# Kernel optimization log

Measured on AMD Instinct MI355X. Metric: run time of the kernel, lower is better.

## Reference

```python
import jax, jax.numpy as jnp
import numpy as np

GRID = (160, 160, 160)
RADIUS_FACTOR = 3.0
PATCH = 20      # fixed patch edge; covers ceil(c+r)-floor(c-r)+1 for r <= 9 voxels
CHUNK = 500
N_POINTS = 25000


def _quat_to_rot(q):
    # normalized quaternion -> rotation matrix (matches torch reference)
    q = q / jnp.clip(jnp.linalg.norm(q, axis=-1, keepdims=True), 1e-6)
    w, x, y, z = q[..., 0], q[..., 1], q[..., 2], q[..., 3]
    ww, xx, yy, zz = w * w, x * x, y * y, z * z
    wx, wy, wz = w * x, w * y, w * z
    xy, xz, yz = x * y, x * z, y * z
    r0 = jnp.stack([ww + xx - yy - zz, 2 * (xy - wz), 2 * (xz + wy)], -1)
    r1 = jnp.stack([2 * (xy + wz), ww - xx + yy - zz, 2 * (yz - wx)], -1)
    r2 = jnp.stack([2 * (xz - wy), 2 * (yz + wx), ww - xx - yy + zz], -1)
    return jnp.stack([r0, r1, r2], -2)


def setup_inputs():
    key = jax.random.key(0)
    k1, k2, k3, k4 = jax.random.split(key, 4)
    centers = jax.random.uniform(k1, (N_POINTS, 3), dtype=jnp.float32)
    # scales in [1.5, 3.0] voxels -> patch radius = 3*max(scale) <= 9 < PATCH/2
    log_scales = jnp.log(jax.random.uniform(k2, (N_POINTS, 3), minval=1.5, maxval=3.0, dtype=jnp.float32))
    quats = jax.random.normal(k3, (N_POINTS, 4), dtype=jnp.float32)
    rho = 0.1 * jax.random.normal(k4, (N_POINTS, 2), dtype=jnp.float32)  # (real, imag)
    return {"centers": centers, "log_scales": log_scales, "quats": quats, "rho": rho}


def _splat(centers, log_scales, quats, rho):
    D, H, W = GRID
    span = jnp.array([D - 1, H - 1, W - 1], jnp.float32)
    scales = jnp.exp(log_scales)                                  # [N,3]
    R = _quat_to_rot(quats)                                       # [N,3,3]
    inv = 1.0 / jnp.clip(scales, 1e-4) ** 2                       # diag of S^-2
    prec = jnp.einsum('nij,nj,nkj->nik', R, inv, R)               # R diag R^T, [N,3,3]
    cv = centers * span                                           # voxel-space centers
    rad = jnp.max(scales, axis=-1) * RADIUS_FACTOR                # per-point patch radius
    base = jnp.floor(cv - rad[:, None]).astype(jnp.int32)         # zmin/ymin/xmin (pre-clip)
    hi = jnp.ceil(cv + rad[:, None]).astype(jnp.int32)            # zmax/ymax/xmax (pre-clip)
    amp_mag = jnp.sqrt(rho[:, 0] ** 2 + rho[:, 1] ** 2)
    valid = (amp_mag >= 1e-6) & (rad >= 1e-3)                     # torch skip conditions
    dims = jnp.array([D, H, W], jnp.int32)

    nchunk = N_POINTS // CHUNK
    ck = lambda a: a.reshape((nchunk, CHUNK) + a.shape[1:])
    xs = (ck(cv), ck(base), ck(hi), ck(prec), ck(rho), ck(valid))
    offs = jnp.arange(PATCH, dtype=jnp.int32)

    def step(vol, x):
        cv_c, base_c, hi_c, p, rho_c, val_c = x
        idx = base_c[:, :, None] + offs                           # [C,3,P] voxel indices
        d = idx.astype(jnp.float32) - cv_c[:, :, None]            # [C,3,P] rel coords
        m = (idx >= 0) & (idx < dims[None, :, None]) & (idx <= hi_c[:, :, None])
        dz, dy, dx = d[:, 0], d[:, 1], d[:, 2]                    # [C,P] each
        # exponent = rel^T prec rel, built separably (prec is symmetric)
        e = ((p[:, 0, 0, None] * dz * dz)[:, :, None, None]
             + (p[:, 1, 1, None] * dy * dy)[:, None, :, None]
             + (p[:, 2, 2, None] * dx * dx)[:, None, None, :]
             + (2.0 * p[:, 0, 1, None, None] * dz[:, :, None] * dy[:, None, :])[:, :, :, None]
             + (2.0 * p[:, 0, 2, None, None] * dz[:, :, None] * dx[:, None, :])[:, :, None, :]
             + (2.0 * p[:, 1, 2, None, None] * dy[:, :, None] * dx[:, None, :])[:, None, :, :])
        w = jnp.exp(-0.5 * e)                                     # [C,P,P,P]
        mask = (m[:, 0, :, None, None] & m[:, 1, None, :, None] & m[:, 2, None, None, :]
                & val_c[:, None, None, None])
        w = jnp.where(mask, w, 0.0)
        iz = jnp.clip(idx[:, 0], 0, D - 1)
        iy = jnp.clip(idx[:, 1], 0, H - 1)
        ix = jnp.clip(idx[:, 2], 0, W - 1)
        lin = (iz[:, :, None, None] * H + iy[:, None, :, None]) * W + ix[:, None, None, :]
        contrib = w[..., None] * rho_c[:, None, None, None, :]    # [C,P,P,P,2] (re,im)
        vol = vol.at[lin.reshape(-1)].add(contrib.reshape(-1, 2))
        return vol, None

    vol, _ = jax.lax.scan(step, jnp.zeros((D * H * W, 2), jnp.float32), xs)
    return vol.reshape(D, H, W, 2)


def reference(centers, log_scales, quats, rho):
    return _splat(centers, log_scales, quats, rho)
```

## Files before the change

kernel.cpp:

```cpp
#include <hip/hip_runtime.h>


namespace {
constexpr int GD = 160, GH = 160, GW = 160;
constexpr int NPTS = 25000;
constexpr int PATCH = 20;
constexpr int TS  = 8;
constexpr int TPD = GD / TS;
constexpr int NT  = TPD * TPD * TPD;
constexpr int CAP = 384;
constexpr int PSTRIDE = 20;
constexpr float L2E = 1.4426950408889634f;
}

typedef float f32x2 __attribute__((ext_vector_type(2)));

__device__ __forceinline__ f32x2 pk_mul(f32x2 a, f32x2 b) {
    f32x2 d;
    asm("v_pk_mul_f32 %0, %1, %2" : "=v"(d) : "v"(a), "v"(b));
    return d;
}
__device__ __forceinline__ f32x2 pk_fma(f32x2 a, f32x2 b, f32x2 c) {
    f32x2 d;
    asm("v_pk_fma_f32 %0, %1, %2, %3" : "=v"(d) : "v"(a), "v"(b), "v"(c));
    return d;
}


__global__ __launch_bounds__(256) void prep_bin(
    const float* __restrict__ centers,
    const float* __restrict__ log_scales,
    const float* __restrict__ quats,
    const float* __restrict__ rho,
    float* __restrict__ params,
    int* __restrict__ counts,
    unsigned short* __restrict__ list)
{
    const int t = blockIdx.x * 256 + threadIdx.x;
    const int gid  = t >> 6;
    const int lane = t & 63;

    const float r0 = rho[gid * 2 + 0];
    const float r1 = rho[gid * 2 + 1];
    const float s0 = __expf(log_scales[gid * 3 + 0]);
    const float s1 = __expf(log_scales[gid * 3 + 1]);
    const float s2 = __expf(log_scales[gid * 3 + 2]);

    const float smax = fmaxf(s0, fmaxf(s1, s2));
    const float rad  = smax * 3.0f;
    const float amp2 = r0 * r0 + r1 * r1;

    const float cvz = centers[gid * 3 + 0] * (float)(GD - 1);
    const float cvy = centers[gid * 3 + 1] * (float)(GH - 1);
    const float cvx = centers[gid * 3 + 2] * (float)(GW - 1);

    const int bz = (int)floorf(cvz - rad);
    const int by = (int)floorf(cvy - rad);
    const int bx = (int)floorf(cvx - rad);
    const int hz = (int)ceilf(cvz + rad);
    const int hy = (int)ceilf(cvy + rad);
    const int hx = (int)ceilf(cvx + rad);

    const int loz = max(bz, 0), upz = min(min(hz, GD - 1), bz + PATCH - 1);
    const int loy = max(by, 0), upy = min(min(hy, GH - 1), by + PATCH - 1);
    const int lox = max(bx, 0), upx = min(min(hx, GW - 1), bx + PATCH - 1);

    const bool valid = (amp2 >= 1e-12f) && (rad >= 1e-3f) &&
                       (upz >= loz) && (upy >= loy) && (upx >= lox);

    const float q0 = quats[gid * 4 + 0], q1 = quats[gid * 4 + 1];
    const float q2 = quats[gid * 4 + 2], q3 = quats[gid * 4 + 3];
    float qn = sqrtf(q0 * q0 + q1 * q1 + q2 * q2 + q3 * q3);
    qn = fmaxf(qn, 1e-6f);
    const float w = q0 / qn, x = q1 / qn, y = q2 / qn, z = q3 / qn;

    const float R00 = w * w + x * x - y * y - z * z;
    const float R01 = 2.f * (x * y - w * z);
    const float R02 = 2.f * (x * z + w * y);
    const float R10 = 2.f * (x * y + w * z);
    const float R11 = w * w - x * x + y * y - z * z;
    const float R12 = 2.f * (y * z - w * x);
    const float R20 = 2.f * (x * z - w * y);
    const float R21 = 2.f * (y * z + w * x);
    const float R22 = w * w - x * x - y * y + z * z;

    const float c0 = fmaxf(s0, 1e-4f); const float i0 = 1.f / (c0 * c0);
    const float c1 = fmaxf(s1, 1e-4f); const float i1 = 1.f / (c1 * c1);
    const float c2 = fmaxf(s2, 1e-4f); const float i2 = 1.f / (c2 * c2);

    const float p00 = R00 * R00 * i0 + R01 * R01 * i1 + R02 * R02 * i2;
    const float p01 = R00 * R10 * i0 + R01 * R11 * i1 + R02 * R12 * i2;
    const float p02 = R00 * R20 * i0 + R01 * R21 * i1 + R02 * R22 * i2;
    const float p11 = R10 * R10 * i0 + R11 * R11 * i1 + R12 * R12 * i2;
    const float p12 = R10 * R20 * i0 + R11 * R21 * i1 + R12 * R22 * i2;
    const float p22 = R20 * R20 * i0 + R21 * R21 * i1 + R22 * R22 * i2;

    const float q00s = -0.5f * L2E * p00;
    const float v    = __builtin_amdgcn_exp2f(2.f * q00s);
    const float v2   = v * v;
    const float v4   = v2 * v2;

    const int zl = valid ? loz : 255, zu = valid ? upz : 0;
    const int yl = valid ? loy : 255, yu = valid ? upy : 0;
    const int xl = valid ? lox : 255, xu = valid ? upx : 0;
    const int loPack = zl | (yl << 8) | (xl << 16) | (zu << 24);
    const int upPack = yu | (xu << 8);

    if (lane == 0) {
        float4* P = reinterpret_cast<float4*>(params + (size_t)gid * PSTRIDE);
        P[0] = make_float4(q00s, -L2E * p01, -L2E * p02, -0.5f * L2E * p11);
        P[1] = make_float4(-L2E * p12, -0.5f * L2E * p22, cvz, cvy);
        P[2] = make_float4(cvx, __int_as_float(loPack), __int_as_float(upPack), v);
        P[3] = make_float4(r0, r0, r1, r1);
        P[4] = make_float4(v2, 0.f, v4, v4);
    }

    if (!valid) return;

    const int tz0 = loz >> 3, tz1 = upz >> 3;
    const int ty0 = loy >> 3, ty1 = upy >> 3;
    const int tx0 = lox >> 3, tx1 = upx >> 3;
    const int tz = tz0 + (lane >> 4);
    const int ty = ty0 + ((lane >> 2) & 3);
    const int tx = tx0 + (lane & 3);
    if (tz > tz1 || ty > ty1 || tx > tx1) return;
    const int tile = (tz * TPD + ty) * TPD + tx;
    const int pos = atomicAdd(&counts[tile], 1);
    if (pos < CAP) list[(size_t)tile * CAP + pos] = (unsigned short)gid;
}

__global__ __launch_bounds__(256, 6) void gather(
    const float* __restrict__ params,
    const int* __restrict__ counts,
    const unsigned short* __restrict__ list,
    float2* __restrict__ out)
{
    const int wli  = threadIdx.x >> 6;
    const int lane = threadIdx.x & 63;
    const int tile = blockIdx.x * 4 + wli;
    const int tz = tile / (TPD * TPD);
    const int rem = tile - tz * (TPD * TPD);
    const int ty = rem / TPD;
    const int tx = rem - ty * TPD;

    const int ly = lane >> 3, lx = lane & 7;
    const int iy = ty * TS + ly;
    const int ix = tx * TS + lx;
    const int z0 = tz * TS;
    const float fy = (float)iy, fx = (float)ix, fz = (float)z0;

    __shared__ float4 sP[4][64][5];

    int cnt = __builtin_amdgcn_readfirstlane(counts[tile]);
    if (cnt > CAP) cnt = CAP;
    const float4* p4 = reinterpret_cast<const float4*>(params);
    const unsigned short* tl = list + (size_t)tile * CAP;

    f32x2 Ar[4], Ai[4];
#pragma unroll
    for (int i = 0; i < 4; ++i) {
        Ar[i].x = 0.f; Ar[i].y = 0.f;
        Ai[i].x = 0.f; Ai[i].y = 0.f;
    }

    for (int b0 = 0; b0 < cnt; b0 += 64) {
        const int nb = min(64, cnt - b0);
        if (lane < nb) {
            const int g = tl[b0 + lane];
            const float4* src = p4 + (size_t)g * 5;
            sP[wli][lane][0] = src[0];
            sP[wli][lane][1] = src[1];
            sP[wli][lane][2] = src[2];
            sP[wli][lane][3] = src[3];
            sP[wli][lane][4] = src[4];
        }
        for (int g = 0; g < nb; ++g) {
            const float4 Pa = sP[wli][g][0];
            const float4 Pb = sP[wli][g][1];
            const float4 Pc = sP[wli][g][2];
            const float4 Pd = sP[wli][g][3];
            const float4 Pe = sP[wli][g][4];
            const int lo = __builtin_amdgcn_readfirstlane(__float_as_int(Pc.y));
            const int up = __builtin_amdgcn_readfirstlane(__float_as_int(Pc.z));
            const int loy_ = (lo >> 8) & 255, lox_ = (lo >> 16) & 255;
            const int upy_ = up & 255,        upx_ = (up >> 8) & 255;
            const int zl = (lo & 255) - z0;
            const int zu = ((lo >> 24) & 255) - z0;
            const bool yx = (iy >= loy_) & (iy <= upy_) &
                            (ix >= lox_) & (ix <= upx_);

            const float dy = fy - Pb.w;
            const float dx = fx - Pc.x;
            const float C = fmaf(dy, fmaf(Pa.w, dy, Pb.x * dx), Pb.y * dx * dx);
            const float B = fmaf(Pa.y, dy, Pa.z * dx);
            const float dz = fz - Pb.z;
            const float t0 = fmaf(dz, fmaf(Pa.x, dz, B), C);
            const float dt = fmaf(Pa.x, fmaf(2.f, dz, 1.f), B);
            const float w0 = __builtin_amdgcn_exp2f(t0);
            const float u0 = __builtin_amdgcn_exp2f(dt);
            const float w0m = yx ? w0 : 0.f;

            const float s0 = u0 * u0 * Pc.w;
            const float s1 = s0 * Pe.x;
            f32x2 W;  W.x = w0m; W.y = w0m * u0;
            f32x2 S;  S.x = s0;  S.y = s1;
            f32x2 R0; R0.x = Pd.x; R0.y = Pd.y;
            f32x2 R1; R1.x = Pd.z; R1.y = Pd.w;
            f32x2 V4; V4.x = Pe.z; V4.y = Pe.w;

            if (zl <= 0 && zu >= 7) {
#pragma unroll
                for (int k = 0; k < 4; ++k) {
                    Ar[k] = pk_fma(W, R0, Ar[k]);
                    Ai[k] = pk_fma(W, R1, Ai[k]);
                    if (k < 3) { W = pk_mul(W, S); S = pk_mul(S, V4); }
                }
            } else {
#pragma unroll
                for (int k = 0; k < 4; ++k) {
                    f32x2 WM;
                    WM.x = (2 * k     >= zl && 2 * k     <= zu) ? W.x : 0.f;
                    WM.y = (2 * k + 1 >= zl && 2 * k + 1 <= zu) ? W.y : 0.f;
                    Ar[k] = pk_fma(WM, R0, Ar[k]);
                    Ai[k] = pk_fma(WM, R1, Ai[k]);
                    if (k < 3) { W = pk_mul(W, S); S = pk_mul(S, V4); }
                }
            }
        }
    }

#pragma unroll
    for (int k = 0; k < 4; ++k) {
        out[((size_t)(z0 + 2 * k)     * GH + iy) * GW + ix] =
            make_float2(Ar[k].x, Ai[k].x);
        out[((size_t)(z0 + 2 * k + 1) * GH + iy) * GW + ix] =
            make_float2(Ar[k].y, Ai[k].y);
    }
}

extern "C" void kernel_launch(void* const* d_in, const int* in_sizes, int n_in,
                              void* d_out, int out_size, void* d_ws, size_t ws_size,
                              hipStream_t stream) {
    const float* centers    = (const float*)d_in[0];
    const float* log_scales = (const float*)d_in[1];
    const float* quats      = (const float*)d_in[2];
    const float* rho        = (const float*)d_in[3];

    float* params = (float*)d_ws;
    int* counts = (int*)(params + (size_t)NPTS * PSTRIDE);
    unsigned short* list = (unsigned short*)(counts + NT);

    hipMemsetAsync(counts, 0, NT * sizeof(int), stream);
    prep_bin<<<(NPTS * 64) / 256, 256, 0, stream>>>(centers, log_scales, quats,
                                                    rho, params, counts, list);
    gather<<<NT / 4, 256, 0, stream>>>(params, counts, list, (float2*)d_out);
}
```

Baseline: 167.7 us.

## Schedule gather tiles via persistent workers pulling heavy tiles first

Adds a small kernel that partitions tiles into a queue, with tiles above a point-count threshold at the front and light tiles at the back. The gather kernel becomes persistent: a fixed grid of waves pulls tiles from the queue with an atomic counter, so heavy tiles start early and light ones fill the tail. This targets load imbalance across tiles with very different list lengths. It costs an extra launch, one global atomic per tile, and an unordered split within each class.

```diff
diff --git a/kernel.cpp b/kernel.cpp
--- a/kernel.cpp
+++ b/kernel.cpp
@@ -10,6 +10,7 @@
 constexpr int NT  = TPD * TPD * TPD;
 constexpr int CAP = 384;
 constexpr int PSTRIDE = 20;
+constexpr int HEAVY_THR = 96;
 constexpr float L2E = 1.4426950408889634f;
 }
 
@@ -129,112 +130,136 @@
     if (pos < CAP) list[(size_t)tile * CAP + pos] = (unsigned short)gid;
 }
 
+__global__ __launch_bounds__(256) void make_queue(
+    const int* __restrict__ counts,
+    int* __restrict__ queue,
+    int* __restrict__ qc)
+{
+    const int t = blockIdx.x * 256 + threadIdx.x;
+    if (t >= NT) return;
+    if (counts[t] > HEAVY_THR) {
+        queue[atomicAdd(&qc[0], 1)] = t;
+    } else {
+        queue[NT - 1 - atomicAdd(&qc[1], 1)] = t;
+    }
+}
+
 __global__ __launch_bounds__(256, 6) void gather(
     const float* __restrict__ params,
     const int* __restrict__ counts,
     const unsigned short* __restrict__ list,
+    const int* __restrict__ queue,
+    int* __restrict__ qc,
     float2* __restrict__ out)
 {
     const int wli  = threadIdx.x >> 6;
     const int lane = threadIdx.x & 63;
-    const int tile = blockIdx.x * 4 + wli;
-    const int tz = tile / (TPD * TPD);
-    const int rem = tile - tz * (TPD * TPD);
-    const int ty = rem / TPD;
-    const int tx = rem - ty * TPD;
-
-    const int ly = lane >> 3, lx = lane & 7;
-    const int iy = ty * TS + ly;
-    const int ix = tx * TS + lx;
-    const int z0 = tz * TS;
-    const float fy = (float)iy, fx = (float)ix, fz = (float)z0;
 
     __shared__ float4 sP[4][64][5];
-
-    int cnt = __builtin_amdgcn_readfirstlane(counts[tile]);
-    if (cnt > CAP) cnt = CAP;
     const float4* p4 = reinterpret_cast<const float4*>(params);
-    const unsigned short* tl = list + (size_t)tile * CAP;
-
-    f32x2 Ar[4], Ai[4];
-#pragma unroll
-    for (int i = 0; i < 4; ++i) {
-        Ar[i].x = 0.f; Ar[i].y = 0.f;
-        Ai[i].x = 0.f; Ai[i].y = 0.f;
-    }
-
-    for (int b0 = 0; b0 < cnt; b0 += 64) {
-        const int nb = min(64, cnt - b0);
-        if (lane < nb) {
-            const int g = tl[b0 + lane];
-            const float4* src = p4 + (size_t)g * 5;
-            sP[wli][lane][0] = src[0];
-            sP[wli][lane][1] = src[1];
-            sP[wli][lane][2] = src[2];
-            sP[wli][lane][3] = src[3];
-            sP[wli][lane][4] = src[4];
+
+    for (;;) {
+        int pos0 = 0;
+        if (lane == 0) pos0 = atomicAdd(&qc[2], 1);
+        const int pos = __shfl(pos0, 0);
+        if (pos >= NT) break;
+        const int tile = __builtin_amdgcn_readfirstlane(queue[pos]);
+
+        const int tz = tile / (TPD * TPD);
+        const int rem = tile - tz * (TPD * TPD);
+        const int ty = rem / TPD;
+        const int tx = rem - ty * TPD;
+
+        const int ly = lane >> 3, lx = lane & 7;
+        const int iy = ty * TS + ly;
+        const int ix = tx * TS + lx;
+        const int z0 = tz * TS;
+        const float fy = (float)iy, fx = (float)ix, fz = (float)z0;
+
+        int cnt = __builtin_amdgcn_readfirstlane(counts[tile]);
+        if (cnt > CAP) cnt = CAP;
+        const unsigned short* tl = list + (size_t)tile * CAP;
+
+        f32x2 Ar[4], Ai[4];
+#pragma unroll
+        for (int i = 0; i < 4; ++i) {
+            Ar[i].x = 0.f; Ar[i].y = 0.f;
+            Ai[i].x = 0.f; Ai[i].y = 0.f;
         }
-        for (int g = 0; g < nb; ++g) {
-            const float4 Pa = sP[wli][g][0];
-            const float4 Pb = sP[wli][g][1];
-            const float4 Pc = sP[wli][g][2];
-            const float4 Pd = sP[wli][g][3];
-            const float4 Pe = sP[wli][g][4];
-            const int lo = __builtin_amdgcn_readfirstlane(__float_as_int(Pc.y));
-            const int up = __builtin_amdgcn_readfirstlane(__float_as_int(Pc.z));
-            const int loy_ = (lo >> 8) & 255, lox_ = (lo >> 16) & 255;
-            const int upy_ = up & 255,        upx_ = (up >> 8) & 255;
-            const int zl = (lo & 255) - z0;
-            const int zu = ((lo >> 24) & 255) - z0;
-            const bool yx = (iy >= loy_) & (iy <= upy_) &
-                            (ix >= lox_) & (ix <= upx_);
-
-            const float dy = fy - Pb.w;
-            const float dx = fx - Pc.x;
-            const float C = fmaf(dy, fmaf(Pa.w, dy, Pb.x * dx), Pb.y * dx * dx);
-            const float B = fmaf(Pa.y, dy, Pa.z * dx);
-            const float dz = fz - Pb.z;
-            const float t0 = fmaf(dz, fmaf(Pa.x, dz, B), C);
-            const float dt = fmaf(Pa.x, fmaf(2.f, dz, 1.f), B);
-            const float w0 = __builtin_amdgcn_exp2f(t0);
-            const float u0 = __builtin_amdgcn_exp2f(dt);
-            const float w0m = yx ? w0 : 0.f;
-
-            const float s0 = u0 * u0 * Pc.w;
-            const float s1 = s0 * Pe.x;
-            f32x2 W;  W.x = w0m; W.y = w0m * u0;
-            f32x2 S;  S.x = s0;  S.y = s1;
-            f32x2 R0; R0.x = Pd.x; R0.y = Pd.y;
-            f32x2 R1; R1.x = Pd.z; R1.y = Pd.w;
-            f32x2 V4; V4.x = Pe.z; V4.y = Pe.w;
-
-            if (zl <= 0 && zu >= 7) {
-#pragma unroll
-                for (int k = 0; k < 4; ++k) {
-                    Ar[k] = pk_fma(W, R0, Ar[k]);
-                    Ai[k] = pk_fma(W, R1, Ai[k]);
-                    if (k < 3) { W = pk_mul(W, S); S = pk_mul(S, V4); }
-                }
-            } else {
-#pragma unroll
-                for (int k = 0; k < 4; ++k) {
-                    f32x2 WM;
-                    WM.x = (2 * k     >= zl && 2 * k     <= zu) ? W.x : 0.f;
-                    WM.y = (2 * k + 1 >= zl && 2 * k + 1 <= zu) ? W.y : 0.f;
-                    Ar[k] = pk_fma(WM, R0, Ar[k]);
-                    Ai[k] = pk_fma(WM, R1, Ai[k]);
-                    if (k < 3) { W = pk_mul(W, S); S = pk_mul(S, V4); }
+
+        for (int b0 = 0; b0 < cnt; b0 += 64) {
+            const int nb = min(64, cnt - b0);
+            if (lane < nb) {
+                const int g = tl[b0 + lane];
+                const float4* src = p4 + (size_t)g * 5;
+                sP[wli][lane][0] = src[0];
+                sP[wli][lane][1] = src[1];
+                sP[wli][lane][2] = src[2];
+                sP[wli][lane][3] = src[3];
+                sP[wli][lane][4] = src[4];
+            }
+            for (int g = 0; g < nb; ++g) {
+                const float4 Pa = sP[wli][g][0];
+                const float4 Pb = sP[wli][g][1];
+                const float4 Pc = sP[wli][g][2];
+                const float4 Pd = sP[wli][g][3];
+                const float4 Pe = sP[wli][g][4];
+                const int lo = __builtin_amdgcn_readfirstlane(__float_as_int(Pc.y));
+                const int up = __builtin_amdgcn_readfirstlane(__float_as_int(Pc.z));
+                const int loy_ = (lo >> 8) & 255, lox_ = (lo >> 16) & 255;
+                const int upy_ = up & 255,        upx_ = (up >> 8) & 255;
+                const int zl = (lo & 255) - z0;
+                const int zu = ((lo >> 24) & 255) - z0;
+                const bool yx = (iy >= loy_) & (iy <= upy_) &
+                                (ix >= lox_) & (ix <= upx_);
+
+                const float dy = fy - Pb.w;
+                const float dx = fx - Pc.x;
+                const float C = fmaf(dy, fmaf(Pa.w, dy, Pb.x * dx), Pb.y * dx * dx);
+                const float B = fmaf(Pa.y, dy, Pa.z * dx);
+                const float dz = fz - Pb.z;
+                const float t0 = fmaf(dz, fmaf(Pa.x, dz, B), C);
+                const float dt = fmaf(Pa.x, fmaf(2.f, dz, 1.f), B);
+                const float w0 = __builtin_amdgcn_exp2f(t0);
+                const float u0 = __builtin_amdgcn_exp2f(dt);
+                const float w0m = yx ? w0 : 0.f;
+
+                const float s0 = u0 * u0 * Pc.w;
+                const float s1 = s0 * Pe.x;
+                f32x2 W;  W.x = w0m; W.y = w0m * u0;
+                f32x2 S;  S.x = s0;  S.y = s1;
+                f32x2 R0; R0.x = Pd.x; R0.y = Pd.y;
+                f32x2 R1; R1.x = Pd.z; R1.y = Pd.w;
+                f32x2 V4; V4.x = Pe.z; V4.y = Pe.w;
+
+                if (zl <= 0 && zu >= 7) {
+#pragma unroll
+                    for (int k = 0; k < 4; ++k) {
+                        Ar[k] = pk_fma(W, R0, Ar[k]);
+                        Ai[k] = pk_fma(W, R1, Ai[k]);
+                        if (k < 3) { W = pk_mul(W, S); S = pk_mul(S, V4); }
+                    }
+                } else {
+#pragma unroll
+                    for (int k = 0; k < 4; ++k) {
+                        f32x2 WM;
+                        WM.x = (2 * k     >= zl && 2 * k     <= zu) ? W.x : 0.f;
+                        WM.y = (2 * k + 1 >= zl && 2 * k + 1 <= zu) ? W.y : 0.f;
+                        Ar[k] = pk_fma(WM, R0, Ar[k]);
+                        Ai[k] = pk_fma(WM, R1, Ai[k]);
+                        if (k < 3) { W = pk_mul(W, S); S = pk_mul(S, V4); }
+                    }
                 }
             }
         }
-    }
-
-#pragma unroll
-    for (int k = 0; k < 4; ++k) {
-        out[((size_t)(z0 + 2 * k)     * GH + iy) * GW + ix] =
-            make_float2(Ar[k].x, Ai[k].x);
-        out[((size_t)(z0 + 2 * k + 1) * GH + iy) * GW + ix] =
-            make_float2(Ar[k].y, Ai[k].y);
+
+#pragma unroll
+        for (int k = 0; k < 4; ++k) {
+            out[((size_t)(z0 + 2 * k)     * GH + iy) * GW + ix] =
+                make_float2(Ar[k].x, Ai[k].x);
+            out[((size_t)(z0 + 2 * k + 1) * GH + iy) * GW + ix] =
+                make_float2(Ar[k].y, Ai[k].y);
+        }
     }
 }
 
@@ -248,10 +273,14 @@
 
     float* params = (float*)d_ws;
     int* counts = (int*)(params + (size_t)NPTS * PSTRIDE);
-    unsigned short* list = (unsigned short*)(counts + NT);
-
-    hipMemsetAsync(counts, 0, NT * sizeof(int), stream);
+    int* qc     = counts + NT;
+    int* queue  = qc + 4;
+    unsigned short* list = (unsigned short*)(queue + NT);
+
+    hipMemsetAsync(counts, 0, (NT + 4) * sizeof(int), stream);
     prep_bin<<<(NPTS * 64) / 256, 256, 0, stream>>>(centers, log_scales, quats,
                                                     rho, params, counts, list);
-    gather<<<NT / 4, 256, 0, stream>>>(params, counts, list, (float2*)d_out);
-}
+    make_queue<<<(NT + 255) / 256, 256, 0, stream>>>(counts, queue, qc);
+    gather<<<2048, 256, 0, stream>>>(params, counts, list, queue, qc,
+                                     (float2*)d_out);
+}
```

Result: slower. 306.2 us (+82.6%).

## Replace LDS staging with register-prefetched uniform param loads in gather

Applied to the files above, without the earlier changes.

Shrinks the per-point parameter record from 20 to 16 floats by dropping duplicated fields. The gather kernel no longer stages batches of parameters in shared memory. Each wave now loads one point's parameters straight from global memory (wave-uniform addresses), with software pipelining that fetches the next point's record and the index after that one while the current point is computed. This removes the LDS writes and reads and the staging phase. The cost is more global/L2 load latency on the critical path and more registers held for the prefetch.

```diff
diff --git a/kernel.cpp b/kernel.cpp
--- a/kernel.cpp
+++ b/kernel.cpp
@@ -9,7 +9,7 @@
 constexpr int TPD = GD / TS;
 constexpr int NT  = TPD * TPD * TPD;
 constexpr int CAP = 384;
-constexpr int PSTRIDE = 20;
+constexpr int PSTRIDE = 16;
 constexpr float L2E = 1.4426950408889634f;
 }
 
@@ -110,9 +110,8 @@
         float4* P = reinterpret_cast<float4*>(params + (size_t)gid * PSTRIDE);
         P[0] = make_float4(q00s, -L2E * p01, -L2E * p02, -0.5f * L2E * p11);
         P[1] = make_float4(-L2E * p12, -0.5f * L2E * p22, cvz, cvy);
-        P[2] = make_float4(cvx, __int_as_float(loPack), __int_as_float(upPack), v);
-        P[3] = make_float4(r0, r0, r1, r1);
-        P[4] = make_float4(v2, 0.f, v4, v4);
+        P[2] = make_float4(cvx, r0, r1, v);
+        P[3] = make_float4(__int_as_float(loPack), __int_as_float(upPack), v2, v4);
     }
 
     if (!valid) return;
@@ -149,8 +148,6 @@
     const int z0 = tz * TS;
     const float fy = (float)iy, fx = (float)ix, fz = (float)z0;
 
-    __shared__ float4 sP[4][64][5];
-
     int cnt = __builtin_amdgcn_readfirstlane(counts[tile]);
     if (cnt > CAP) cnt = CAP;
     const float4* p4 = reinterpret_cast<const float4*>(params);
@@ -163,25 +160,24 @@
         Ai[i].x = 0.f; Ai[i].y = 0.f;
     }
 
-    for (int b0 = 0; b0 < cnt; b0 += 64) {
-        const int nb = min(64, cnt - b0);
-        if (lane < nb) {
-            const int g = tl[b0 + lane];
-            const float4* src = p4 + (size_t)g * 5;
-            sP[wli][lane][0] = src[0];
-            sP[wli][lane][1] = src[1];
-            sP[wli][lane][2] = src[2];
-            sP[wli][lane][3] = src[3];
-            sP[wli][lane][4] = src[4];
-        }
-        for (int g = 0; g < nb; ++g) {
-            const float4 Pa = sP[wli][g][0];
-            const float4 Pb = sP[wli][g][1];
-            const float4 Pc = sP[wli][g][2];
-            const float4 Pd = sP[wli][g][3];
-            const float4 Pe = sP[wli][g][4];
-            const int lo = __builtin_amdgcn_readfirstlane(__float_as_int(Pc.y));
-            const int up = __builtin_amdgcn_readfirstlane(__float_as_int(Pc.z));
+    if (cnt > 0) {
+        int gidA = __builtin_amdgcn_readfirstlane(tl[0]);
+        float4 Pa = p4[(size_t)gidA * 4 + 0];
+        float4 Pb = p4[(size_t)gidA * 4 + 1];
+        float4 Pc = p4[(size_t)gidA * 4 + 2];
+        float4 Pd = p4[(size_t)gidA * 4 + 3];
+        int gidB = __builtin_amdgcn_readfirstlane(tl[cnt > 1 ? 1 : 0]);
+
+        for (int g = 0; g < cnt; ++g) {
+            const int gidC = __builtin_amdgcn_readfirstlane(
+                tl[min(g + 2, cnt - 1)]);
+            const float4 Qa = p4[(size_t)gidB * 4 + 0];
+            const float4 Qb = p4[(size_t)gidB * 4 + 1];
+            const float4 Qc = p4[(size_t)gidB * 4 + 2];
+            const float4 Qd = p4[(size_t)gidB * 4 + 3];
+
+            const int lo = __builtin_amdgcn_readfirstlane(__float_as_int(Pd.x));
+            const int up = __builtin_amdgcn_readfirstlane(__float_as_int(Pd.y));
             const int loy_ = (lo >> 8) & 255, lox_ = (lo >> 16) & 255;
             const int upy_ = up & 255,        upx_ = (up >> 8) & 255;
             const int zl = (lo & 255) - z0;
@@ -201,12 +197,12 @@
             const float w0m = yx ? w0 : 0.f;
 
             const float s0 = u0 * u0 * Pc.w;
-            const float s1 = s0 * Pe.x;
+            const float s1 = s0 * Pd.z;
             f32x2 W;  W.x = w0m; W.y = w0m * u0;
             f32x2 S;  S.x = s0;  S.y = s1;
-            f32x2 R0; R0.x = Pd.x; R0.y = Pd.y;
-            f32x2 R1; R1.x = Pd.z; R1.y = Pd.w;
-            f32x2 V4; V4.x = Pe.z; V4.y = Pe.w;
+            f32x2 R0; R0.x = Pc.y; R0.y = Pc.y;
+            f32x2 R1; R1.x = Pc.z; R1.y = Pc.z;
+            f32x2 V4; V4.x = Pd.w; V4.y = Pd.w;
 
             if (zl <= 0 && zu >= 7) {
 #pragma unroll
@@ -226,6 +222,9 @@
                     if (k < 3) { W = pk_mul(W, S); S = pk_mul(S, V4); }
                 }
             }
+
+            Pa = Qa; Pb = Qb; Pc = Qc; Pd = Qd;
+            gidB = gidC;
         }
     }
 
```

Result: slower. 171.1 us (+2.0%).

## Prefetch per-Gaussian params into scalar registers and process two tiles per wave

Applied to the files above, without the earlier changes.

The gather kernel stops staging Gaussian parameters through LDS. It now loads them with wave-uniform indices, so they can live in scalar registers, and software-pipelines the loads two Gaussians ahead. The per-lane yx bounds test becomes a wave-uniform 64-bit lane mask consumed by v_cndmask, and the packed FMAs take SGPR operands. Each wave now handles two tiles, halving the grid. The aims are to remove LDS traffic and barriers and to cut VALU work, at the risk of scalar-load latency stalls and less parallelism.

```diff
diff --git a/kernel.cpp b/kernel.cpp
--- a/kernel.cpp
+++ b/kernel.cpp
@@ -10,6 +10,8 @@
 constexpr int NT  = TPD * TPD * TPD;
 constexpr int CAP = 384;
 constexpr int PSTRIDE = 20;
+constexpr int TPW = 2;
+constexpr int NWAVE = NT / TPW;
 constexpr float L2E = 1.4426950408889634f;
 }
 
@@ -20,9 +22,14 @@
     asm("v_pk_mul_f32 %0, %1, %2" : "=v"(d) : "v"(a), "v"(b));
     return d;
 }
-__device__ __forceinline__ f32x2 pk_fma(f32x2 a, f32x2 b, f32x2 c) {
+__device__ __forceinline__ f32x2 pk_mul_s(f32x2 a, f32x2 b_s) {
     f32x2 d;
-    asm("v_pk_fma_f32 %0, %1, %2, %3" : "=v"(d) : "v"(a), "v"(b), "v"(c));
+    asm("v_pk_mul_f32 %0, %1, %2" : "=v"(d) : "v"(a), "s"(b_s));
+    return d;
+}
+__device__ __forceinline__ f32x2 pk_fma_s(f32x2 a, f32x2 b_s, f32x2 c) {
+    f32x2 d;
+    asm("v_pk_fma_f32 %0, %1, %2, %3" : "=v"(d) : "v"(a), "s"(b_s), "v"(c));
     return d;
 }
 
@@ -137,104 +144,135 @@
 {
     const int wli  = threadIdx.x >> 6;
     const int lane = threadIdx.x & 63;
-    const int tile = blockIdx.x * 4 + wli;
-    const int tz = tile / (TPD * TPD);
-    const int rem = tile - tz * (TPD * TPD);
-    const int ty = rem / TPD;
-    const int tx = rem - ty * TPD;
-
+    const int wid  = blockIdx.x * 4 + wli;
     const int ly = lane >> 3, lx = lane & 7;
-    const int iy = ty * TS + ly;
-    const int ix = tx * TS + lx;
-    const int z0 = tz * TS;
-    const float fy = (float)iy, fx = (float)ix, fz = (float)z0;
-
-    __shared__ float4 sP[4][64][5];
-
-    int cnt = __builtin_amdgcn_readfirstlane(counts[tile]);
-    if (cnt > CAP) cnt = CAP;
     const float4* p4 = reinterpret_cast<const float4*>(params);
-    const unsigned short* tl = list + (size_t)tile * CAP;
-
-    f32x2 Ar[4], Ai[4];
-#pragma unroll
-    for (int i = 0; i < 4; ++i) {
-        Ar[i].x = 0.f; Ar[i].y = 0.f;
-        Ai[i].x = 0.f; Ai[i].y = 0.f;
-    }
-
-    for (int b0 = 0; b0 < cnt; b0 += 64) {
-        const int nb = min(64, cnt - b0);
-        if (lane < nb) {
-            const int g = tl[b0 + lane];
-            const float4* src = p4 + (size_t)g * 5;
-            sP[wli][lane][0] = src[0];
-            sP[wli][lane][1] = src[1];
-            sP[wli][lane][2] = src[2];
-            sP[wli][lane][3] = src[3];
-            sP[wli][lane][4] = src[4];
+
+    for (int tt = 0; tt < TPW; ++tt) {
+        const int tile = __builtin_amdgcn_readfirstlane(wid + tt * NWAVE);
+        const int tz = tile / (TPD * TPD);
+        const int rem = tile - tz * (TPD * TPD);
+        const int ty = rem / TPD;
+        const int tx = rem - ty * TPD;
+
+        const int iy = ty * TS + ly;
+        const int ix = tx * TS + lx;
+        const int z0 = tz * TS;
+        const float fy = (float)iy, fx = (float)ix, fz = (float)z0;
+
+        int cnt = __builtin_amdgcn_readfirstlane(counts[tile]);
+        if (cnt > CAP) cnt = CAP;
+        const unsigned short* tl = list + (size_t)tile * CAP;
+
+        f32x2 Ar[4], Ai[4];
+#pragma unroll
+        for (int i = 0; i < 4; ++i) {
+            Ar[i].x = 0.f; Ar[i].y = 0.f;
+            Ai[i].x = 0.f; Ai[i].y = 0.f;
         }
-        for (int g = 0; g < nb; ++g) {
-            const float4 Pa = sP[wli][g][0];
-            const float4 Pb = sP[wli][g][1];
-            const float4 Pc = sP[wli][g][2];
-            const float4 Pd = sP[wli][g][3];
-            const float4 Pe = sP[wli][g][4];
-            const int lo = __builtin_amdgcn_readfirstlane(__float_as_int(Pc.y));
-            const int up = __builtin_amdgcn_readfirstlane(__float_as_int(Pc.z));
-            const int loy_ = (lo >> 8) & 255, lox_ = (lo >> 16) & 255;
-            const int upy_ = up & 255,        upx_ = (up >> 8) & 255;
-            const int zl = (lo & 255) - z0;
-            const int zu = ((lo >> 24) & 255) - z0;
-            const bool yx = (iy >= loy_) & (iy <= upy_) &
-                            (ix >= lox_) & (ix <= upx_);
-
-            const float dy = fy - Pb.w;
-            const float dx = fx - Pc.x;
-            const float C = fmaf(dy, fmaf(Pa.w, dy, Pb.x * dx), Pb.y * dx * dx);
-            const float B = fmaf(Pa.y, dy, Pa.z * dx);
-            const float dz = fz - Pb.z;
-            const float t0 = fmaf(dz, fmaf(Pa.x, dz, B), C);
-            const float dt = fmaf(Pa.x, fmaf(2.f, dz, 1.f), B);
-            const float w0 = __builtin_amdgcn_exp2f(t0);
-            const float u0 = __builtin_amdgcn_exp2f(dt);
-            const float w0m = yx ? w0 : 0.f;
-
-            const float s0 = u0 * u0 * Pc.w;
-            const float s1 = s0 * Pe.x;
-            f32x2 W;  W.x = w0m; W.y = w0m * u0;
-            f32x2 S;  S.x = s0;  S.y = s1;
-            f32x2 R0; R0.x = Pd.x; R0.y = Pd.y;
-            f32x2 R1; R1.x = Pd.z; R1.y = Pd.w;
-            f32x2 V4; V4.x = Pe.z; V4.y = Pe.w;
-
-            if (zl <= 0 && zu >= 7) {
-#pragma unroll
-                for (int k = 0; k < 4; ++k) {
-                    Ar[k] = pk_fma(W, R0, Ar[k]);
-                    Ai[k] = pk_fma(W, R1, Ai[k]);
-                    if (k < 3) { W = pk_mul(W, S); S = pk_mul(S, V4); }
+
+        if (cnt > 0) {
+            int gidA = __builtin_amdgcn_readfirstlane(tl[0]);
+            float4 Pa = p4[(size_t)gidA * 5 + 0];
+            float4 Pb = p4[(size_t)gidA * 5 + 1];
+            float4 Pc = p4[(size_t)gidA * 5 + 2];
+            float4 Pd = p4[(size_t)gidA * 5 + 3];
+            float4 Pe = p4[(size_t)gidA * 5 + 4];
+            int gidB = __builtin_amdgcn_readfirstlane(tl[cnt > 1 ? 1 : 0]);
+
+            for (int g = 0; g < cnt; ++g) {
+                const int gidC = __builtin_amdgcn_readfirstlane(
+                    tl[min(g + 2, cnt - 1)]);
+                const float4 Qa = p4[(size_t)gidB * 5 + 0];
+                const float4 Qb = p4[(size_t)gidB * 5 + 1];
+                const float4 Qc = p4[(size_t)gidB * 5 + 2];
+                const float4 Qd = p4[(size_t)gidB * 5 + 3];
+                const float4 Qe = p4[(size_t)gidB * 5 + 4];
+
+                const int lo = __builtin_amdgcn_readfirstlane(
+                    __float_as_int(Pc.y));
+                const int up = __builtin_amdgcn_readfirstlane(
+                    __float_as_int(Pc.z));
+                const int loy_ = (lo >> 8) & 255, lox_ = (lo >> 16) & 255;
+                const int upy_ = up & 255,        upx_ = (up >> 8) & 255;
+                const int zl = (lo & 255) - z0;
+                const int zu = ((lo >> 24) & 255) - z0;
+
+                const int ylc = min(max(loy_ - ty * TS, 0), 8);
+                const int yuc = min(max(upy_ - ty * TS, -1), 7);
+                const int xlc = min(max(lox_ - tx * TS, 0), 8);
+                const int xuc = min(max(upx_ - tx * TS, -1), 7);
+                unsigned long long mask = 0ULL;
+                if (yuc >= ylc && xuc >= xlc) {
+                    const unsigned colb =
+                        ((0xFFu << xlc) & (0xFFu >> (7 - xuc))) & 0xFFu;
+                    const unsigned c4 = colb * 0x01010101u;
+                    const unsigned long long col8 =
+                        ((unsigned long long)c4 << 32) | c4;
+                    const unsigned long long rowm =
+                        (~0ULL >> (8 * (7 - yuc))) & (~0ULL << (8 * ylc));
+                    mask = col8 & rowm;
                 }
-            } else {
-#pragma unroll
-                for (int k = 0; k < 4; ++k) {
-                    f32x2 WM;
-                    WM.x = (2 * k     >= zl && 2 * k     <= zu) ? W.x : 0.f;
-                    WM.y = (2 * k + 1 >= zl && 2 * k + 1 <= zu) ? W.y : 0.f;
-                    Ar[k] = pk_fma(WM, R0, Ar[k]);
-                    Ai[k] = pk_fma(WM, R1, Ai[k]);
-                    if (k < 3) { W = pk_mul(W, S); S = pk_mul(S, V4); }
+                const unsigned mlo = __builtin_amdgcn_readfirstlane(
+                    (unsigned)mask);
+                const unsigned mhi = __builtin_amdgcn_readfirstlane(
+                    (unsigned)(mask >> 32));
+                const unsigned long long msk =
+                    ((unsigned long long)mhi << 32) | mlo;
+
+                const float dy = fy - Pb.w;
+                const float dx = fx - Pc.x;
+                const float C = fmaf(dy, fmaf(Pa.w, dy, Pb.x * dx),
+                                     Pb.y * dx * dx);
+                const float B = fmaf(Pa.y, dy, Pa.z * dx);
+                const float dz = fz - Pb.z;
+                const float t0 = fmaf(dz, fmaf(Pa.x, dz, B), C);
+                const float dt = fmaf(Pa.x, fmaf(2.f, dz, 1.f), B);
+                const float w0 = __builtin_amdgcn_exp2f(t0);
+                const float u0 = __builtin_amdgcn_exp2f(dt);
+                float w0m;
+                asm("v_cndmask_b32 %0, 0, %1, %2"
+                    : "=v"(w0m) : "v"(w0), "s"(msk));
+
+                const float s0 = u0 * u0 * Pc.w;
+                const float s1 = s0 * Pe.x;
+                f32x2 W;  W.x = w0m; W.y = w0m * u0;
+                f32x2 S;  S.x = s0;  S.y = s1;
+                f32x2 R0; R0.x = Pd.x; R0.y = Pd.y;
+                f32x2 R1; R1.x = Pd.z; R1.y = Pd.w;
+                f32x2 V4; V4.x = Pe.z; V4.y = Pe.w;
+
+                if (zl <= 0 && zu >= 7) {
+#pragma unroll
+                    for (int k = 0; k < 4; ++k) {
+                        Ar[k] = pk_fma_s(W, R0, Ar[k]);
+                        Ai[k] = pk_fma_s(W, R1, Ai[k]);
+                        if (k < 3) { W = pk_mul(W, S); S = pk_mul_s(S, V4); }
+                    }
+                } else {
+#pragma unroll
+                    for (int k = 0; k < 4; ++k) {
+                        f32x2 WM;
+                        WM.x = (2 * k     >= zl && 2 * k     <= zu) ? W.x : 0.f;
+                        WM.y = (2 * k + 1 >= zl && 2 * k + 1 <= zu) ? W.y : 0.f;
+                        Ar[k] = pk_fma_s(WM, R0, Ar[k]);
+                        Ai[k] = pk_fma_s(WM, R1, Ai[k]);
+                        if (k < 3) { W = pk_mul(W, S); S = pk_mul_s(S, V4); }
+                    }
                 }
+
+                Pa = Qa; Pb = Qb; Pc = Qc; Pd = Qd; Pe = Qe;
+                gidB = gidC;
             }
         }
-    }
-
-#pragma unroll
-    for (int k = 0; k < 4; ++k) {
-        out[((size_t)(z0 + 2 * k)     * GH + iy) * GW + ix] =
-            make_float2(Ar[k].x, Ai[k].x);
-        out[((size_t)(z0 + 2 * k + 1) * GH + iy) * GW + ix] =
-            make_float2(Ar[k].y, Ai[k].y);
+
+#pragma unroll
+        for (int k = 0; k < 4; ++k) {
+            out[((size_t)(z0 + 2 * k)     * GH + iy) * GW + ix] =
+                make_float2(Ar[k].x, Ai[k].x);
+            out[((size_t)(z0 + 2 * k + 1) * GH + iy) * GW + ix] =
+                make_float2(Ar[k].y, Ai[k].y);
+        }
     }
 }
 
@@ -250,8 +288,8 @@
     int* counts = (int*)(params + (size_t)NPTS * PSTRIDE);
     unsigned short* list = (unsigned short*)(counts + NT);
 
-    hipMemsetAsync(counts, 0, NT * sizeof(int), stream);
+    (void)hipMemsetAsync(counts, 0, NT * sizeof(int), stream);
     prep_bin<<<(NPTS * 64) / 256, 256, 0, stream>>>(centers, log_scales, quats,
                                                     rho, params, counts, list);
-    gather<<<NT / 4, 256, 0, stream>>>(params, counts, list, (float2*)d_out);
-}
+    gather<<<NWAVE / 4, 256, 0, stream>>>(params, counts, list, (float2*)d_out);
+}
```

Result: slower. 227.9 us (+35.9%).
